# Kernel optimization log

Measured on AMD Instinct MI355X. Metric: run time of the kernel, lower is better.

The kernel has to match this reference:

```python
import jax, jax.numpy as jnp
import numpy as np

B, C, H, W, K = 16, 256, 64, 64, 31
PAD = K // 2
EPS = 1e-5


def setup_inputs() -> dict:
    key = jax.random.key(0)
    k1, k2, k3 = jax.random.split(key, 3)
    x = jax.random.normal(k1, (B, C, H, W), dtype=jnp.float32)
    dw_w = jax.random.normal(k2, (C, 1, K, K), dtype=jnp.float32) * 0.02
    pw_w = jax.random.normal(k3, (C, C), dtype=jnp.float32) * 0.05
    gamma = jnp.ones((C,), dtype=jnp.float32)
    beta = jnp.zeros((C,), dtype=jnp.float32)
    return {"x": x, "dw_w": dw_w, "gamma": gamma, "beta": beta, "pw_w": pw_w}


def reference(x, dw_w, gamma, beta, pw_w):
    # depthwise 31x31 conv, padding=15, groups=C
    y = jax.lax.conv_general_dilated(
        x, dw_w,
        window_strides=(1, 1),
        padding=[(PAD, PAD), (PAD, PAD)],
        dimension_numbers=("NCHW", "OIHW", "NCHW"),
        feature_group_count=C,
    )
    # BatchNorm2d in training mode: biased batch stats over (N,H,W)
    mean = jnp.mean(y, axis=(0, 2, 3), keepdims=True)
    var = jnp.var(y, axis=(0, 2, 3), keepdims=True)  # biased, as torch uses for normalization
    g = gamma[None, :, None, None]
    b = beta[None, :, None, None]
    yn = (y - mean) * jax.lax.rsqrt(var + EPS) * g + b
    r = jax.nn.relu(yn)
    # pointwise 1x1 conv == channel-mixing matmul
    out = jnp.einsum("oc,bchw->bohw", pw_w, r)
    return out
```

## Files before the change

### kernel.cpp

```cpp
#include <hip/hip_runtime.h>
#include <hip/hip_bf16.h>

namespace {
constexpr int CB   = 256;
constexpr int HWp  = 4096;
constexpr int NB   = 16;

typedef __bf16    bf16x8 __attribute__((ext_vector_type(8)));
typedef float     f32x4  __attribute__((ext_vector_type(4)));
typedef float     f32x16 __attribute__((ext_vector_type(16)));
typedef _Float16  f16x2  __attribute__((ext_vector_type(2)));
typedef _Float16  f16x8  __attribute__((ext_vector_type(8)));

typedef __attribute__((address_space(1))) void gvoid;
typedef __attribute__((address_space(3))) void svoid;

__device__ __forceinline__ unsigned int pack2(float lo, float hi) {
#if __has_builtin(__builtin_amdgcn_cvt_pkrtz)
    return __builtin_bit_cast(unsigned int, __builtin_amdgcn_cvt_pkrtz(lo, hi));
#else
    f16x2 v; v[0] = (_Float16)lo; v[1] = (_Float16)hi;
    return __builtin_bit_cast(unsigned int, v);
#endif
}

constexpr int TOEP_PER_C = 31 * 4 * 64;
constexpr int HALO_U32   = 94 * 64;
}

__global__ __launch_bounds__(256) void prep_kernel(
    const float* __restrict__ pw, __hip_bfloat16* __restrict__ pwb,
    const float* __restrict__ dw, uint4* __restrict__ toep)
{
    const int bid = blockIdx.x;
    const int tid = threadIdx.x;
    if (bid < 64) {
        const int idx = bid * 256 + tid;
        const float4 v = reinterpret_cast<const float4*>(pw)[idx];
        union { __hip_bfloat16 h[4]; uint2 u; } pk;
        pk.h[0] = __float2bfloat16(v.x); pk.h[1] = __float2bfloat16(v.y);
        pk.h[2] = __float2bfloat16(v.z); pk.h[3] = __float2bfloat16(v.w);
        reinterpret_cast<uint2*>(pwb)[idx] = pk.u;
        return;
    }
    const int flat = (bid - 64) * 256 + tid;
    const int lane = flat & 63;
    const int kq   = (flat >> 6) & 3;
    const int rc   = flat >> 8;
    const int r    = rc % 31;
    const int c    = rc / 31;
    const int i    = lane & 31;
    const int kbase = kq * 16 + (lane >> 5) * 8;

    const float* __restrict__ wr = dw + (size_t)c * 961 + r * 31;
    union { _Float16 h[8]; uint4 u; } out;
#pragma unroll
    for (int e = 0; e < 8; ++e) {
        const int t = kbase + e - i - 1;
        out.h[e] = (t >= 0 && t <= 30) ? (_Float16)wr[t] : (_Float16)0.f;
    }
    toep[flat] = out.u;
}

__global__ __launch_bounds__(256, 3) void dwconv_kernel(
    const float* __restrict__ x, const uint4* __restrict__ toep,
    _Float16* __restrict__ y16, float* __restrict__ gsum, float* __restrict__ gsumsq)
{
    __shared__ unsigned int xs[2 * HALO_U32];

    const int bid = blockIdx.x;
    const int c   = bid & 255;
    const int bp  = bid >> 8;
    const int tid = threadIdx.x;

    for (int idx = tid; idx < 2 * HALO_U32 / 4; idx += 256)
        reinterpret_cast<uint4*>(xs)[idx] = uint4{0, 0, 0, 0};
    __syncthreads();

    {
        const int row = tid >> 2;
        const int q   = tid & 3;
        const int hr  = row + 15;
        const int swz = (hr & 7) << 2;
        const int p0  = (8  + q * 8) ^ swz;
        const int p1  = (12 + q * 8) ^ swz;
#pragma unroll
        for (int img = 0; img < 2; ++img) {
            const float4* src = reinterpret_cast<const float4*>(
                x + ((size_t)((bp * 2 + img) * CB + c)) * HWp + row * 64 + q * 16);
            float4 v0 = src[0], v1 = src[1], v2 = src[2], v3 = src[3];
            uint4 a, b;
            a.x = pack2(v0.x, v0.y); a.y = pack2(v0.z, v0.w);
            a.z = pack2(v1.x, v1.y); a.w = pack2(v1.z, v1.w);
            b.x = pack2(v2.x, v2.y); b.y = pack2(v2.z, v2.w);
            b.z = pack2(v3.x, v3.y); b.w = pack2(v3.z, v3.w);
            unsigned int* base = xs + img * HALO_U32 + hr * 64;
            *reinterpret_cast<uint4*>(base + p0) = a;
            *reinterpret_cast<uint4*>(base + p1) = b;
        }
    }
    __syncthreads();

    const int lane = tid & 63;
    const int wid  = tid >> 6;
    const int j    = lane & 31;
    const int half = lane >> 5;
    const int rowb = wid * 16 + (j >> 1);
    const int colb = (j & 1) * 16 + half * 4;
    const uint4* __restrict__ tp = toep + (size_t)c * TOEP_PER_C + lane;

    f32x16 acc0 = {}, acc1 = {};
    uint4 afA[4];
#pragma unroll
    for (int kq = 0; kq < 4; ++kq) afA[kq] = tp[kq * 64];

#pragma unroll 1
    for (int r = 0; r < 31; ++r) {
        uint4 afB[4];
        if (r < 30) {
#pragma unroll
            for (int kq = 0; kq < 4; ++kq) afB[kq] = tp[((r + 1) * 4 + kq) * 64];
        }
        const int row = rowb + r;
        const int swz = (row & 7) << 2;
        const unsigned int* __restrict__ xr = xs + row * 64;
        f16x8 b0[4], b1[4];
#pragma unroll
        for (int kq = 0; kq < 4; ++kq) {
            const int p = (colb + kq * 8) ^ swz;
            b0[kq] = *reinterpret_cast<const f16x8*>(xr + p);
            b1[kq] = *reinterpret_cast<const f16x8*>(xr + HALO_U32 + p);
        }
#pragma unroll
        for (int kq = 0; kq < 4; ++kq)
            acc0 = __builtin_amdgcn_mfma_f32_32x32x16_f16(
                __builtin_bit_cast(f16x8, afA[kq]), b0[kq], acc0, 0, 0, 0);
#pragma unroll
        for (int kq = 0; kq < 4; ++kq)
            acc1 = __builtin_amdgcn_mfma_f32_32x32x16_f16(
                __builtin_bit_cast(f16x8, afA[kq]), b1[kq], acc1, 0, 0, 0);
        if (r < 30) {
#pragma unroll
            for (int kq = 0; kq < 4; ++kq) afA[kq] = afB[kq];
        }
    }

    const size_t pl0 = ((size_t)(bp * 2 * CB + c)) * HWp + rowb * 64 + (j & 1) * 32 + 4 * half;
#pragma unroll
    for (int g = 0; g < 4; ++g) {
        uint2 u0, u1;
        u0.x = pack2(acc0[4 * g + 0], acc0[4 * g + 1]);
        u0.y = pack2(acc0[4 * g + 2], acc0[4 * g + 3]);
        u1.x = pack2(acc1[4 * g + 0], acc1[4 * g + 1]);
        u1.y = pack2(acc1[4 * g + 2], acc1[4 * g + 3]);
        *reinterpret_cast<uint2*>(y16 + pl0 + 8 * g)            = u0;
        *reinterpret_cast<uint2*>(y16 + pl0 + CB * HWp + 8 * g) = u1;
    }

    float s = 0.f, s2 = 0.f;
#pragma unroll
    for (int t = 0; t < 16; ++t) {
        s += acc0[t] + acc1[t];
        s2 = fmaf(acc0[t], acc0[t], s2);
        s2 = fmaf(acc1[t], acc1[t], s2);
    }
#pragma unroll
    for (int off = 32; off > 0; off >>= 1) {
        s  += __shfl_down(s,  off, 64);
        s2 += __shfl_down(s2, off, 64);
    }
    if (lane == 0) {
        atomicAdd(&gsum[c],   s);
        atomicAdd(&gsumsq[c], s2);
    }
}

__global__ __launch_bounds__(256) void normtrans_kernel(
    const _Float16* __restrict__ y16,
    const float* __restrict__ gsum, const float* __restrict__ gsumsq,
    const float* __restrict__ gamma, const float* __restrict__ beta,
    __hip_bfloat16* __restrict__ rt)
{
    __shared__ __hip_bfloat16 tile[32 * 72];
    __shared__ float scsh[64];
    const int b   = blockIdx.z;
    const int c0  = blockIdx.y * 32;
    const int p0  = blockIdx.x * 64;
    const int tid = threadIdx.x;

    const int cl  = tid >> 3;
    const int pl8 = (tid & 7) * 8;
    const uint4 raw = *reinterpret_cast<const uint4*>(
        y16 + ((size_t)(b * CB + c0 + cl)) * HWp + p0 + pl8);
    if (tid < 32) {
        const int cc = c0 + tid;
        const float inv = 1.f / 65536.f;
        const float mean = gsum[cc] * inv;
        const float var  = gsumsq[cc] * inv - mean * mean;
        const float sc   = gamma[cc] * rsqrtf(var + 1e-5f);
        scsh[tid]      = sc;
        scsh[32 + tid] = beta[cc] - mean * sc;
    }
    __syncthreads();
    {
        const float sc = scsh[cl], sh = scsh[32 + cl];
        const f16x8 hv = __builtin_bit_cast(f16x8, raw);
        union { __hip_bfloat16 h[8]; uint4 u; } o;
#pragma unroll
        for (int e = 0; e < 8; ++e)
            o.h[e] = __float2bfloat16(fmaxf(fmaf((float)hv[e], sc, sh), 0.f));
        *reinterpret_cast<uint4*>(&tile[cl * 72 + pl8]) = o.u;
    }
    __syncthreads();
    {
        const int pl  = tid >> 2;
        const int cl8 = (tid & 3) * 8;
        union { __hip_bfloat16 h[8]; uint4 u; } o;
#pragma unroll
        for (int e = 0; e < 8; ++e) o.h[e] = tile[(cl8 + e) * 72 + pl];
        *reinterpret_cast<uint4*>(
            rt + ((size_t)b * HWp + p0 + pl) * CB + c0 + cl8) = o.u;
    }
}

__global__ __launch_bounds__(256, 2) void gemm_kernel(
    const __hip_bfloat16* __restrict__ pwb, const __hip_bfloat16* __restrict__ rt,
    float* __restrict__ out)
{
    __shared__ __hip_bfloat16 ldsA[128 * 32];
    __shared__ __hip_bfloat16 ldsB[128 * 32];

    const int tid  = threadIdx.x;
    const int lane = tid & 63;
    const int wid  = tid >> 6;
    const int b    = blockIdx.z;
    const int m0   = blockIdx.y * 128;
    const int p0   = blockIdx.x * 128;
    const int wm   = wid >> 1, wn = wid & 1;

    f32x4 acc[4][4];
#pragma unroll
    for (int mi = 0; mi < 4; ++mi)
#pragma unroll
        for (int ni = 0; ni < 4; ++ni) acc[mi][ni] = {0.f, 0.f, 0.f, 0.f};

    const int srow = lane >> 2;
    const int scol = (lane & 3) * 8;
    const int fr   = lane & 15;
    const int fk   = (lane >> 4) * 8;

    const size_t rtbase = (size_t)b * HWp;

    for (int ks = 0; ks < 8; ++ks) {
        const int k0 = ks * 32;
#pragma unroll
        for (int q = 0; q < 2; ++q) {
            const int issue = wid * 2 + q;
            const int row   = issue * 16 + srow;
            const __hip_bfloat16* gA = pwb + (size_t)(m0 + row) * CB + k0 + scol;
            const __hip_bfloat16* gB = rt + (rtbase + p0 + row) * CB + k0 + scol;
            __builtin_amdgcn_global_load_lds((gvoid*)gA, (svoid*)(ldsA + issue * 512), 16, 0, 0);
            __builtin_amdgcn_global_load_lds((gvoid*)gB, (svoid*)(ldsB + issue * 512), 16, 0, 0);
        }
        __syncthreads();

        bf16x8 af[4], bfr[4];
#pragma unroll
        for (int mi = 0; mi < 4; ++mi)
            af[mi] = *reinterpret_cast<const bf16x8*>(
                ldsA + (wm * 64 + mi * 16 + fr) * 32 + fk);
#pragma unroll
        for (int ni = 0; ni < 4; ++ni)
            bfr[ni] = *reinterpret_cast<const bf16x8*>(
                ldsB + (wn * 64 + ni * 16 + fr) * 32 + fk);

#pragma unroll
        for (int mi = 0; mi < 4; ++mi)
#pragma unroll
            for (int ni = 0; ni < 4; ++ni)
                acc[mi][ni] = __builtin_amdgcn_mfma_f32_16x16x32_bf16(
                    af[mi], bfr[ni], acc[mi][ni], 0, 0, 0);
        __syncthreads();
    }

    const int frow = (lane >> 4) * 4;
#pragma unroll
    for (int mi = 0; mi < 4; ++mi)
#pragma unroll
        for (int ni = 0; ni < 4; ++ni)
#pragma unroll
            for (int v = 0; v < 4; ++v) {
                const int o = m0 + wm * 64 + mi * 16 + frow + v;
                const int p = p0 + wn * 64 + ni * 16 + fr;
                out[((size_t)(b * CB + o)) * HWp + p] = acc[mi][ni][v];
            }
}

extern "C" void kernel_launch(void* const* d_in, const int* in_sizes, int n_in,
                              void* d_out, int out_size, void* d_ws, size_t ws_size,
                              hipStream_t stream) {
    (void)in_sizes; (void)n_in; (void)out_size; (void)ws_size;
    const float* x     = (const float*)d_in[0];
    const float* dw    = (const float*)d_in[1];
    const float* gamma = (const float*)d_in[2];
    const float* beta  = (const float*)d_in[3];
    const float* pw    = (const float*)d_in[4];
    float* out = (float*)d_out;

    char* ws = (char*)d_ws;
    uint4* toep        = (uint4*)ws;
    __hip_bfloat16* rt = (__hip_bfloat16*)ws;
    float* gsum   = (float*)(ws + (size_t)33554432);
    float* gsumsq = gsum + 256;
    __hip_bfloat16* pwb = (__hip_bfloat16*)(ws + (size_t)33554432 + 4096);

    _Float16* y16 = (_Float16*)d_out;

    hipMemsetAsync(gsum, 0, 2048, stream);

    prep_kernel<<<dim3(8000), 256, 0, stream>>>(pw, pwb, dw, toep);
    dwconv_kernel<<<dim3(2048), 256, 0, stream>>>(x, toep, y16, gsum, gsumsq);
    normtrans_kernel<<<dim3(64, 8, NB), 256, 0, stream>>>(y16, gsum, gsumsq,
                                                          gamma, beta, rt);
    gemm_kernel<<<dim3(32, 2, NB), 256, 0, stream>>>(pwb, rt, out);
}
```

Measured before the change: 219.8 us.

## Fuse BN-normalize/ReLU/transpose into GEMM B-tile load and double-buffer A

Removes the separate normalize-and-transpose kernel. The GEMM now reads the fp16 depthwise output directly, applies the batch-norm scale/shift and ReLU per channel, and writes the transposed bf16 tile into LDS. The A operand is double-buffered with one barrier per k-step. The stats memset is folded into the prep kernel, and buffers are reassigned so the Toeplitz weights sit in the output buffer. This saves a full intermediate write/read and a launch, at the cost of strided 2-byte LDS stores and more per-block ALU work.

```diff
diff --git a/kernel.cpp b/kernel.cpp
--- a/kernel.cpp
+++ b/kernel.cpp
@@ -30,11 +30,13 @@
 
 __global__ __launch_bounds__(256) void prep_kernel(
     const float* __restrict__ pw, __hip_bfloat16* __restrict__ pwb,
-    const float* __restrict__ dw, uint4* __restrict__ toep)
+    const float* __restrict__ dw, uint4* __restrict__ toep,
+    float* __restrict__ gsum)
 {
     const int bid = blockIdx.x;
     const int tid = threadIdx.x;
     if (bid < 64) {
+        if (bid == 0) { gsum[tid] = 0.f; gsum[256 + tid] = 0.f; }
         const int idx = bid * 256 + tid;
         const float4 v = reinterpret_cast<const float4*>(pw)[idx];
         union { __hip_bfloat16 h[4]; uint2 u; } pk;
@@ -175,60 +177,15 @@
     }
 }
 
-__global__ __launch_bounds__(256) void normtrans_kernel(
-    const _Float16* __restrict__ y16,
+__global__ __launch_bounds__(256, 4) void gemm_kernel(
+    const __hip_bfloat16* __restrict__ pwb, const _Float16* __restrict__ y16,
     const float* __restrict__ gsum, const float* __restrict__ gsumsq,
     const float* __restrict__ gamma, const float* __restrict__ beta,
-    __hip_bfloat16* __restrict__ rt)
-{
-    __shared__ __hip_bfloat16 tile[32 * 72];
-    __shared__ float scsh[64];
-    const int b   = blockIdx.z;
-    const int c0  = blockIdx.y * 32;
-    const int p0  = blockIdx.x * 64;
-    const int tid = threadIdx.x;
-
-    const int cl  = tid >> 3;
-    const int pl8 = (tid & 7) * 8;
-    const uint4 raw = *reinterpret_cast<const uint4*>(
-        y16 + ((size_t)(b * CB + c0 + cl)) * HWp + p0 + pl8);
-    if (tid < 32) {
-        const int cc = c0 + tid;
-        const float inv = 1.f / 65536.f;
-        const float mean = gsum[cc] * inv;
-        const float var  = gsumsq[cc] * inv - mean * mean;
-        const float sc   = gamma[cc] * rsqrtf(var + 1e-5f);
-        scsh[tid]      = sc;
-        scsh[32 + tid] = beta[cc] - mean * sc;
-    }
-    __syncthreads();
-    {
-        const float sc = scsh[cl], sh = scsh[32 + cl];
-        const f16x8 hv = __builtin_bit_cast(f16x8, raw);
-        union { __hip_bfloat16 h[8]; uint4 u; } o;
-#pragma unroll
-        for (int e = 0; e < 8; ++e)
-            o.h[e] = __float2bfloat16(fmaxf(fmaf((float)hv[e], sc, sh), 0.f));
-        *reinterpret_cast<uint4*>(&tile[cl * 72 + pl8]) = o.u;
-    }
-    __syncthreads();
-    {
-        const int pl  = tid >> 2;
-        const int cl8 = (tid & 3) * 8;
-        union { __hip_bfloat16 h[8]; uint4 u; } o;
-#pragma unroll
-        for (int e = 0; e < 8; ++e) o.h[e] = tile[(cl8 + e) * 72 + pl];
-        *reinterpret_cast<uint4*>(
-            rt + ((size_t)b * HWp + p0 + pl) * CB + c0 + cl8) = o.u;
-    }
-}
-
-__global__ __launch_bounds__(256, 2) void gemm_kernel(
-    const __hip_bfloat16* __restrict__ pwb, const __hip_bfloat16* __restrict__ rt,
     float* __restrict__ out)
 {
-    __shared__ __hip_bfloat16 ldsA[128 * 32];
-    __shared__ __hip_bfloat16 ldsB[128 * 32];
+    __shared__ __hip_bfloat16 ldsA[2][128 * 32];
+    __shared__ unsigned short  ldsB[2][128 * 32];
+    __shared__ float scsh[512];
 
     const int tid  = threadIdx.x;
     const int lane = tid & 63;
@@ -238,6 +195,15 @@
     const int p0   = blockIdx.x * 128;
     const int wm   = wid >> 1, wn = wid & 1;
 
+    {
+        const float inv = 1.f / 65536.f;
+        const float mean = gsum[tid] * inv;
+        const float var  = gsumsq[tid] * inv - mean * mean;
+        const float sc   = gamma[tid] * rsqrtf(var + 1e-5f);
+        scsh[tid]       = sc;
+        scsh[256 + tid] = beta[tid] - mean * sc;
+    }
+
     f32x4 acc[4][4];
 #pragma unroll
     for (int mi = 0; mi < 4; ++mi)
@@ -248,39 +214,74 @@
     const int scol = (lane & 3) * 8;
     const int fr   = lane & 15;
     const int fk   = (lane >> 4) * 8;
-
-    const size_t rtbase = (size_t)b * HWp;
+    const int cb   = tid & 31;
+    const int pg   = tid >> 5;
+
+    const _Float16* __restrict__ yb =
+        y16 + ((size_t)b * CB + cb) * HWp + p0 + pg * 16;
+
+    uint4 ya0 = *reinterpret_cast<const uint4*>(yb);
+    uint4 ya1 = *reinterpret_cast<const uint4*>(yb + 8);
+#pragma unroll
+    for (int q = 0; q < 2; ++q) {
+        const int issue = wid * 2 + q;
+        const int row   = issue * 16 + srow;
+        __builtin_amdgcn_global_load_lds(
+            (gvoid*)(pwb + (size_t)(m0 + row) * CB + scol),
+            (svoid*)(&ldsA[0][issue * 512]), 16, 0, 0);
+    }
+    __syncthreads();
 
     for (int ks = 0; ks < 8; ++ks) {
-        const int k0 = ks * 32;
-#pragma unroll
-        for (int q = 0; q < 2; ++q) {
-            const int issue = wid * 2 + q;
-            const int row   = issue * 16 + srow;
-            const __hip_bfloat16* gA = pwb + (size_t)(m0 + row) * CB + k0 + scol;
-            const __hip_bfloat16* gB = rt + (rtbase + p0 + row) * CB + k0 + scol;
-            __builtin_amdgcn_global_load_lds((gvoid*)gA, (svoid*)(ldsA + issue * 512), 16, 0, 0);
-            __builtin_amdgcn_global_load_lds((gvoid*)gB, (svoid*)(ldsB + issue * 512), 16, 0, 0);
+        const int cur = ks & 1;
+        const float scv = scsh[ks * 32 + cb];
+        const float shv = scsh[256 + ks * 32 + cb];
+        const f16x8 h0 = __builtin_bit_cast(f16x8, ya0);
+        const f16x8 h1 = __builtin_bit_cast(f16x8, ya1);
+        unsigned short rb[16];
+#pragma unroll
+        for (int e = 0; e < 8; ++e) {
+            const __hip_bfloat16 v0 = __float2bfloat16(fmaxf(fmaf((float)h0[e], scv, shv), 0.f));
+            const __hip_bfloat16 v1 = __float2bfloat16(fmaxf(fmaf((float)h1[e], scv, shv), 0.f));
+            rb[e]     = __builtin_bit_cast(unsigned short, v0);
+            rb[8 + e] = __builtin_bit_cast(unsigned short, v1);
+        }
+        unsigned short* bw = &ldsB[cur][(pg * 16) * 32 + cb];
+#pragma unroll
+        for (int e = 0; e < 16; ++e) bw[e * 32] = rb[e];
+
+        if (ks < 7) {
+            const _Float16* yn = yb + (size_t)(ks + 1) * 32 * HWp;
+            ya0 = *reinterpret_cast<const uint4*>(yn);
+            ya1 = *reinterpret_cast<const uint4*>(yn + 8);
+            const int k0 = (ks + 1) * 32;
+#pragma unroll
+            for (int q = 0; q < 2; ++q) {
+                const int issue = wid * 2 + q;
+                const int row   = issue * 16 + srow;
+                __builtin_amdgcn_global_load_lds(
+                    (gvoid*)(pwb + (size_t)(m0 + row) * CB + k0 + scol),
+                    (svoid*)(&ldsA[cur ^ 1][issue * 512]), 16, 0, 0);
+            }
         }
         __syncthreads();
 
-        bf16x8 af[4], bfr[4];
+        bf16x8 af[4], bfv[4];
 #pragma unroll
         for (int mi = 0; mi < 4; ++mi)
             af[mi] = *reinterpret_cast<const bf16x8*>(
-                ldsA + (wm * 64 + mi * 16 + fr) * 32 + fk);
+                &ldsA[cur][(wm * 64 + mi * 16 + fr) * 32 + fk]);
 #pragma unroll
         for (int ni = 0; ni < 4; ++ni)
-            bfr[ni] = *reinterpret_cast<const bf16x8*>(
-                ldsB + (wn * 64 + ni * 16 + fr) * 32 + fk);
+            bfv[ni] = *reinterpret_cast<const bf16x8*>(
+                &ldsB[cur][(wn * 64 + ni * 16 + fr) * 32 + fk]);
 
 #pragma unroll
         for (int mi = 0; mi < 4; ++mi)
 #pragma unroll
             for (int ni = 0; ni < 4; ++ni)
                 acc[mi][ni] = __builtin_amdgcn_mfma_f32_16x16x32_bf16(
-                    af[mi], bfr[ni], acc[mi][ni], 0, 0, 0);
-        __syncthreads();
+                    af[mi], bfv[ni], acc[mi][ni], 0, 0, 0);
     }
 
     const int frow = (lane >> 4) * 4;
@@ -308,19 +309,14 @@
     float* out = (float*)d_out;
 
     char* ws = (char*)d_ws;
-    uint4* toep        = (uint4*)ws;
-    __hip_bfloat16* rt = (__hip_bfloat16*)ws;
+    uint4* toep   = (uint4*)d_out;
+    _Float16* y16 = (_Float16*)ws;
     float* gsum   = (float*)(ws + (size_t)33554432);
     float* gsumsq = gsum + 256;
     __hip_bfloat16* pwb = (__hip_bfloat16*)(ws + (size_t)33554432 + 4096);
 
-    _Float16* y16 = (_Float16*)d_out;
-
-    hipMemsetAsync(gsum, 0, 2048, stream);
-
-    prep_kernel<<<dim3(8000), 256, 0, stream>>>(pw, pwb, dw, toep);
+    prep_kernel<<<dim3(8000), 256, 0, stream>>>(pw, pwb, dw, toep, gsum);
     dwconv_kernel<<<dim3(2048), 256, 0, stream>>>(x, toep, y16, gsum, gsumsq);
-    normtrans_kernel<<<dim3(64, 8, NB), 256, 0, stream>>>(y16, gsum, gsumsq,
-                                                          gamma, beta, rt);
-    gemm_kernel<<<dim3(32, 2, NB), 256, 0, stream>>>(pwb, rt, out);
-}
+    gemm_kernel<<<dim3(32, 2, NB), 256, 0, stream>>>(pwb, y16, gsum, gsumsq,
+                                                     gamma, beta, out);
+}
```

New measurement: 205.3 us. 6.6% less time.
